# Performance work log

Hardware: AMD Instinct MI355X
Metric: run time of the kernel (lower is better)

The kernel has to match this reference:

```python
import jax, jax.numpy as jnp
from jax import lax
import numpy as np

LEVEL_HW = [(100, 100), (50, 50), (25, 25), (13, 13), (7, 7)]  # P3..P7 for 800x800 input
N, C, A, K, NCONV = 2, 256, 9, 80, 4
PRIOR_PROB = 0.01


def conv3x3(x, w, b):
    # x: (N,C,H,W), w: (O,I,3,3), stride 1, pad 1
    y = lax.conv_general_dilated(x, w, (1, 1), 'SAME',
                                 dimension_numbers=('NCHW', 'OIHW', 'NCHW'))
    return y + b[None, :, None, None]


def permute_to_N_HWA_K(t, k):
    # (N, A*k, H, W) -> (N, H*W*A, k), matching the torch helper
    n, _, h, w = t.shape
    return t.reshape(n, -1, k, h, w).transpose(0, 3, 4, 1, 2).reshape(n, -1, k)


def setup_inputs() -> dict:
    key = jax.random.key(0)
    ks = iter(jax.random.split(key, 64))
    inp = {}
    for i, (h, w) in enumerate(LEVEL_HW):
        inp[f"f{i}"] = jax.random.normal(next(ks), (N, C, h, w), jnp.float32)
    for pre in ("cls", "box"):
        for i in range(NCONV):
            inp[f"{pre}_w{i}"] = 0.01 * jax.random.normal(next(ks), (C, C, 3, 3), jnp.float32)
            inp[f"{pre}_b{i}"] = jnp.zeros((C,), jnp.float32)
    bias_value = -float(np.log((1.0 - PRIOR_PROB) / PRIOR_PROB))
    inp["cls_score_w"] = 0.01 * jax.random.normal(next(ks), (A * K, C, 3, 3), jnp.float32)
    inp["cls_score_b"] = jnp.full((A * K,), bias_value, jnp.float32)
    inp["box_pred_w"] = 0.01 * jax.random.normal(next(ks), (A * 4, C, 3, 3), jnp.float32)
    inp["box_pred_b"] = jnp.zeros((A * 4,), jnp.float32)
    return inp


def reference(f0, f1, f2, f3, f4,
              cls_w0, cls_b0, cls_w1, cls_b1, cls_w2, cls_b2, cls_w3, cls_b3,
              box_w0, box_b0, box_w1, box_b1, box_w2, box_b2, box_w3, box_b3,
              cls_score_w, cls_score_b, box_pred_w, box_pred_b):
    feats = [f0, f1, f2, f3, f4]
    cls_p = [(cls_w0, cls_b0), (cls_w1, cls_b1), (cls_w2, cls_b2), (cls_w3, cls_b3)]
    box_p = [(box_w0, box_b0), (box_w1, box_b1), (box_w2, box_b2), (box_w3, box_b3)]
    logits, boxes = [], []
    for f in feats:
        x = f
        for w, b in cls_p:
            x = jax.nn.relu(conv3x3(x, w, b))
        logits.append(permute_to_N_HWA_K(conv3x3(x, cls_score_w, cls_score_b), K))
        y = f
        for w, b in box_p:
            y = jax.nn.relu(conv3x3(y, w, b))
        boxes.append(permute_to_N_HWA_K(conv3x3(y, box_pred_w, box_pred_b), 4))
    # (N, R, K) and (N, R, 4) with R = sum_l Hl*Wl*A = 120087; concat on last dim
    return jnp.concatenate([jnp.concatenate(logits, 1), jnp.concatenate(boxes, 1)], axis=2)
```

## Files before the change

kernel.cpp:

```cpp
#include <hip/hip_runtime.h>


typedef __attribute__((ext_vector_type(8))) short short8;
typedef __attribute__((ext_vector_type(4))) float floatx4;

#define LVLTOT 14143

__device__ __forceinline__ unsigned short f2bf(float f) {
  unsigned int u = __float_as_uint(f);
  unsigned int r = (u + 0x7fffu + ((u >> 16) & 1u)) >> 16;
  return (unsigned short)r;
}

__device__ __forceinline__ void gload_lds16(const void* g, void* l) {
  __builtin_amdgcn_global_load_lds(
      (const __attribute__((address_space(1))) unsigned int*)g,
      (__attribute__((address_space(3))) unsigned int*)l, 16, 0, 0);
}

struct PrepArgs {
  const float* f[5];
  const float* w[10];
  unsigned short* wdst[10];
  int wblk_off[11];
  int cout[10];
  unsigned short* x0;
  unsigned short* bufA;
  unsigned short* bufB;
};

__global__ __launch_bounds__(256) void prep(PrepArgs A) {
  static const int Ht[5] = {100, 50, 25, 13, 7};
  static const int Wpt[5] = {102, 52, 27, 15, 9};
  static const int LOFFt[5] = {0, 10404, 13108, 13837, 14062};
  __shared__ float ts[32][33];
  const int bid = blockIdx.x;
  const int t = threadIdx.x;

  if (bid < 1090) {
    int sid = bid % 545, n = bid / 545;
    int l, h, wb;
    if (sid < 400)      { l = 0; h = sid >> 2; wb = sid & 3; }
    else if (sid < 500) { l = 1; h = (sid - 400) >> 1; wb = (sid - 400) & 1; }
    else if (sid < 525) { l = 2; h = sid - 500; wb = 0; }
    else if (sid < 538) { l = 3; h = sid - 525; wb = 0; }
    else                { l = 4; h = sid - 538; wb = 0; }
    const float* f = A.f[l];
    int H = Ht[l], W = H, Wp = Wpt[l], loff = LOFFt[l];
    int w0 = wb * 32;
    for (int s = 0; s < 8; s++) {
      int ch0 = s * 32;
      __syncthreads();
#pragma unroll
      for (int r4 = 0; r4 < 4; r4++) {
        int ch = ch0 + (t >> 5) + r4 * 8;
        int px = w0 + (t & 31);
        float v = 0.f;
        if (px < W) v = f[(((size_t)n * 256 + ch) * H + h) * W + px];
        ts[(t >> 5) + r4 * 8][t & 31] = v;
      }
      __syncthreads();
      int pxl = t >> 3, c4 = t & 7;
      if (w0 + pxl < W) {
        unsigned short pk[4];
#pragma unroll
        for (int k = 0; k < 4; k++) pk[k] = f2bf(ts[c4 * 4 + k][pxl]);
        *(unsigned long long*)(A.x0 +
            ((size_t)n * LVLTOT + loff + (size_t)(h + 1) * Wp + (w0 + pxl + 1)) *
                256 + ch0 + c4 * 4) = *(unsigned long long*)pk;
      }
    }
    return;
  }

  if (bid < 3970) {
    int b2 = bid - 1090;
    int tix = 0;
    while (b2 >= A.wblk_off[tix + 1]) tix++;
    int co = b2 - A.wblk_off[tix];
    int ci = t;
    bool valid = co < A.cout[tix];
    const float* w = A.w[tix];
    unsigned short* dst = A.wdst[tix];
    int cb = co >> 6, col = co & 63, chk = ci >> 5, qd = (ci >> 3) & 3, j = ci & 7;
#pragma unroll
    for (int tap = 0; tap < 9; tap++) {
      float v = valid ? w[((size_t)co * 256 + ci) * 9 + tap] : 0.f;
      dst[((((size_t)(cb * 8 + chk) * 9 + tap) * 4 + qd) * 64 + col) * 8 + j] =
          f2bf(v);
    }
    return;
  }

  {
    static const int BCUM[6] = {0, 404, 608, 712, 768, 800};
    int b3 = bid - 3970;
    int plane = b3 / 100;
    int item = (b3 % 100) * 256 + t;
    int pxi = item >> 5, oct = item & 31;
    if (pxi >= 800) return;
    int l = 0;
    while (pxi >= BCUM[l + 1]) l++;
    int j = pxi - BCUM[l];
    int Wp = Wpt[l];
    int r, c;
    if (j < Wp)            { r = 0; c = j; }
    else if (j < 2 * Wp)   { r = Wp - 1; c = j - Wp; }
    else { int k = j - 2 * Wp; r = 1 + (k >> 1); c = (k & 1) ? Wp - 1 : 0; }
    size_t px = (size_t)LOFFt[l] + (size_t)r * Wp + c;
    unsigned short* base = (plane < 4)
                               ? (A.bufA + (size_t)plane * LVLTOT * 256)
                               : (A.bufB + (size_t)(plane - 4) * LVLTOT * 256);
    floatx4 z;
    z[0] = z[1] = z[2] = z[3] = 0.f;
    *(floatx4*)(base + px * 256 + oct * 8) = z;
  }
}

__device__ __forceinline__ void decode_tile(int tile, int& l, int& h0, int& w0,
                                            int& H, int& W, int& Wp, int& loff) {
  const int Ht[5] = {100, 50, 25, 13, 7};
  const int Wpt[5] = {102, 52, 27, 15, 9};
  const int TXt[5] = {7, 4, 2, 1, 1};
  const int LOFFt[5] = {0, 10404, 13108, 13837, 14062};
  int tloc;
  if (tile < 49) { l = 0; tloc = tile; }
  else if (tile < 65) { l = 1; tloc = tile - 49; }
  else if (tile < 69) { l = 2; tloc = tile - 65; }
  else if (tile < 70) { l = 3; tloc = tile - 69; }
  else { l = 4; tloc = 0; }
  H = Ht[l]; W = H; Wp = Wpt[l]; loff = LOFFt[l];
  int ty = tloc / TXt[l], tx = tloc - ty * TXt[l];
  h0 = ty * 16; w0 = tx * 16;
}

#define CONV_MAIN_LOOP(INP, WBLOB, CB)                                         \
  {                                                                            \
    size_t xoff[6];                                                            \
    _Pragma("unroll") for (int g = 0; g < 6; g++) {                            \
      int px = g * 64 + lane;                                                  \
      int r = px / 18, c = px - r * 18;                                        \
      int hh = h0 + r; if (hh > Hpad - 1) hh = Hpad - 1;                       \
      int ww = w0 + c; if (ww > Wp - 1) ww = Wp - 1;                           \
      xoff[g] = ((size_t)hh * Wp + ww) * 256 + wv * 8;                         \
    }                                                                          \
    for (int ch = 0; ch < 8; ch++) {                                           \
      if (ch) __syncthreads();                                                 \
      const unsigned short* wsrc = (WBLOB) + ((size_t)((CB)*8 + ch)) * 18432;  \
      _Pragma("unroll") for (int i = 0; i < 9; i++)                            \
        gload_lds16(wsrc + i * 2048 + wv * 512 + lane * 8,                     \
                    lds_w + i * 2048 + wv * 512);                              \
      _Pragma("unroll") for (int g = 0; g < 6; g++)                            \
        gload_lds16((INP) + xoff[g] + ch * 32, lds_x + wv * 3072 + g * 512);   \
      __syncthreads();                                                         \
      const short8* xw = (const short8*)lds_w;                                 \
      const short8* xx = (const short8*)lds_x;                                 \
      _Pragma("unroll") for (int tdx = 0; tdx < 3; tdx++) {                    \
        short8 bfr[6];                                                         \
        _Pragma("unroll") for (int rw = 0; rw < 6; rw++)                       \
          bfr[rw] = xx[q * 384 + (wv * 4 + rw) * 18 + n16 + tdx];              \
        _Pragma("unroll") for (int tdy = 0; tdy < 3; tdy++) {                  \
          const int tap = tdy * 3 + tdx;                                       \
          _Pragma("unroll") for (int cc = 0; cc < 4; cc++) {                   \
            short8 afr = xw[(tap * 4 + q) * 64 + cc * 16 + n16];               \
            _Pragma("unroll") for (int rr = 0; rr < 4; rr++)                   \
              acc[cc][rr] = __builtin_amdgcn_mfma_f32_16x16x32_bf16(           \
                  afr, bfr[rr + tdy], acc[cc][rr], 0, 0, 0);                   \
          }                                                                    \
        }                                                                      \
      }                                                                        \
    }                                                                          \
  }

__global__ __launch_bounds__(256, 2) void conv_tower_mfma(
    const unsigned short* __restrict__ xin, unsigned short* __restrict__ xout,
    const unsigned short* __restrict__ wblob_cls,
    const unsigned short* __restrict__ wblob_box,
    const float* __restrict__ bias_cls, const float* __restrict__ bias_box,
    int in_n_stride, int in_tw_stride) {
  __shared__ __align__(16) unsigned short lds_w[18432];
  __shared__ __align__(16) unsigned short lds_x[12288];
  const int t = threadIdx.x, lane = t & 63, wv = t >> 6;
  const int q = lane >> 4, n16 = lane & 15;
  int l, h0, w0, H, W, Wp, loff;
  decode_tile(blockIdx.x, l, h0, w0, H, W, Wp, loff);
  const int Hpad = H + 2;
  const int cb = blockIdx.y;
  const int n = blockIdx.z >> 1, tw = blockIdx.z & 1;
  const unsigned short* wblob = tw ? wblob_box : wblob_cls;
  const float* bias = tw ? bias_box : bias_cls;
  const unsigned short* inp =
      xin + ((size_t)n * in_n_stride + (size_t)tw * in_tw_stride + loff) * 256;
  unsigned short* outp = xout + ((size_t)(n * 2 + tw) * LVLTOT + loff) * 256;

  floatx4 acc[4][4];
#pragma unroll
  for (int i = 0; i < 4; i++)
#pragma unroll
    for (int jj = 0; jj < 4; jj++) acc[i][jj] = (floatx4){0.f, 0.f, 0.f, 0.f};

  CONV_MAIN_LOOP(inp, wblob, cb)

#pragma unroll
  for (int cc = 0; cc < 4; cc++) {
    floatx4 bb = *(const floatx4*)(bias + cb * 64 + cc * 16 + q * 4);
#pragma unroll
    for (int rr = 0; rr < 4; rr++) {
      int h = h0 + wv * 4 + rr;
      int w_ = w0 + n16;
      if (h < H && w_ < W) {
        unsigned short pk[4];
#pragma unroll
        for (int rg = 0; rg < 4; rg++)
          pk[rg] = f2bf(fmaxf(acc[cc][rr][rg] + bb[rg], 0.f));
        size_t base =
            ((size_t)(h + 1) * Wp + (w_ + 1)) * 256 + cb * 64 + cc * 16 + q * 4;
        *(unsigned long long*)(outp + base) = *(unsigned long long*)pk;
      }
    }
  }
}

__global__ __launch_bounds__(256, 2) void conv_final_mfma(
    const unsigned short* __restrict__ xin, float* __restrict__ out,
    const unsigned short* __restrict__ wblob_cls,
    const unsigned short* __restrict__ wblob_box,
    const float* __restrict__ bias_cls, const float* __restrict__ bias_box) {
  __shared__ __align__(16) unsigned short lds_w[18432];
  __shared__ __align__(16) unsigned short lds_x[12288];
  const int t = threadIdx.x, lane = t & 63, wv = t >> 6;
  const int q = lane >> 4, n16 = lane & 15;
  int l, h0, w0, H, W, Wp, loff;
  decode_tile(blockIdx.x, l, h0, w0, H, W, Wp, loff);
  const int Hpad = H + 2;
  const int yb = blockIdx.y;
  const bool is_cls = yb < 12;
  const int cb = is_cls ? yb : 0;
  const int tw = is_cls ? 0 : 1;
  const int Cout = is_cls ? 720 : 36;
  const unsigned short* wblob = is_cls ? wblob_cls : wblob_box;
  const float* bias = is_cls ? bias_cls : bias_box;
  const int n = blockIdx.z;
  const int RB[5] = {0, 90000, 112500, 118125, 119646};
  const unsigned short* inp = xin + ((size_t)(n * 2 + tw) * LVLTOT + loff) * 256;

  floatx4 acc[4][4];
#pragma unroll
  for (int i = 0; i < 4; i++)
#pragma unroll
    for (int jj = 0; jj < 4; jj++) acc[i][jj] = (floatx4){0.f, 0.f, 0.f, 0.f};

  CONV_MAIN_LOOP(inp, wblob, cb)

#pragma unroll
  for (int cc = 0; cc < 4; cc++) {
    int co0 = cb * 64 + cc * 16 + q * 4;
    if (co0 >= Cout) continue;
    floatx4 bb = *(const floatx4*)(bias + co0);
    int a = is_cls ? (co0 / 80) : (co0 >> 2);
    int col0 = is_cls ? (co0 - a * 80) : 80;
#pragma unroll
    for (int rr = 0; rr < 4; rr++) {
      int h = h0 + wv * 4 + rr;
      int w_ = w0 + n16;
      if (h < H && w_ < W) {
        size_t ridx = (size_t)RB[l] + ((size_t)h * W + w_) * 9 + a;
        floatx4 v;
#pragma unroll
        for (int rg = 0; rg < 4; rg++) v[rg] = acc[cc][rr][rg] + bb[rg];
        *(floatx4*)(out + ((size_t)n * 120087 + ridx) * 84 + col0) = v;
      }
    }
  }
}

extern "C" void kernel_launch(void* const* d_in, const int* in_sizes, int n_in,
                              void* d_out, int out_size, void* d_ws,
                              size_t ws_size, hipStream_t stream) {
  char* ws = (char*)d_ws;
  unsigned short* bufB = (unsigned short*)(ws);
  unsigned short* X0 = (unsigned short*)(ws + 14482432);
  unsigned short* bufA = (unsigned short*)(ws + 28964864);
  unsigned short* tb[8];
  for (int i = 0; i < 8; i++)
    tb[i] = (unsigned short*)(ws + 57929728 + (size_t)i * 1179648);
  unsigned short* fb_cls = (unsigned short*)(ws + 67366912);
  unsigned short* fb_box = (unsigned short*)(ws + 70905856);

  float* out = (float*)d_out;

  PrepArgs pa;
  for (int i = 0; i < 5; i++) pa.f[i] = (const float*)d_in[i];
  for (int i = 0; i < 4; i++) {
    pa.w[i] = (const float*)d_in[5 + 2 * i];
    pa.w[4 + i] = (const float*)d_in[13 + 2 * i];
    pa.wdst[i] = tb[i];
    pa.wdst[4 + i] = tb[4 + i];
    pa.cout[i] = pa.cout[4 + i] = 256;
  }
  pa.w[8] = (const float*)d_in[21]; pa.wdst[8] = fb_cls; pa.cout[8] = 720;
  pa.w[9] = (const float*)d_in[23]; pa.wdst[9] = fb_box; pa.cout[9] = 36;
  int off = 0;
  for (int i = 0; i < 8; i++) { pa.wblk_off[i] = off; off += 256; }
  pa.wblk_off[8] = off; off += 768;
  pa.wblk_off[9] = off; off += 64;
  pa.wblk_off[10] = off;
  pa.x0 = X0;
  pa.bufA = bufA;
  pa.bufB = bufB;

  prep<<<dim3(4770), 256, 0, stream>>>(pa);

  const float *cls_b[4], *box_b[4];
  for (int i = 0; i < 4; i++) {
    cls_b[i] = (const float*)d_in[6 + 2 * i];
    box_b[i] = (const float*)d_in[14 + 2 * i];
  }

  dim3 gt(71, 4, 4);
  conv_tower_mfma<<<gt, 256, 0, stream>>>(X0, bufA, tb[0], tb[4], cls_b[0],
                                          box_b[0], LVLTOT, 0);
  conv_tower_mfma<<<gt, 256, 0, stream>>>(bufA, bufB, tb[1], tb[5], cls_b[1],
                                          box_b[1], 2 * LVLTOT, LVLTOT);
  conv_tower_mfma<<<gt, 256, 0, stream>>>(bufB, bufA, tb[2], tb[6], cls_b[2],
                                          box_b[2], 2 * LVLTOT, LVLTOT);
  conv_tower_mfma<<<gt, 256, 0, stream>>>(bufA, bufB, tb[3], tb[7], cls_b[3],
                                          box_b[3], 2 * LVLTOT, LVLTOT);

  conv_final_mfma<<<dim3(71, 13, 2), 256, 0, stream>>>(
      bufB, out, fb_cls, fb_box, (const float*)d_in[22], (const float*)d_in[24]);
}
```

Measured before the change: 638.5 us.

## Tile convs as packed 2x16 row segments across levels to cut padding waste

Replaces the fixed 16x16 spatial tiles per level with 2-row by 16-column segments. Each block packs 8 such segments, which can come from different pyramid levels, so partially empty tiles on the small levels and edges waste less compute. The input halo tile grows to 4x18 per segment, meaning each segment loads 72 pixels for 32 outputs. This raises LDS input usage and per-thread address setup, and the halo reuse is worse than with 16x16 tiles.

Measured after the change: 632.2 us. No clear change (-1.0%).

```diff
diff --git a/kernel.cpp b/kernel.cpp
--- a/kernel.cpp
+++ b/kernel.cpp
@@ -117,55 +117,62 @@
   }
 }
 
-__device__ __forceinline__ void decode_tile(int tile, int& l, int& h0, int& w0,
-                                            int& H, int& W, int& Wp, int& loff) {
-  const int Ht[5] = {100, 50, 25, 13, 7};
-  const int Wpt[5] = {102, 52, 27, 15, 9};
-  const int TXt[5] = {7, 4, 2, 1, 1};
-  const int LOFFt[5] = {0, 10404, 13108, 13837, 14062};
-  int tloc;
-  if (tile < 49) { l = 0; tloc = tile; }
-  else if (tile < 65) { l = 1; tloc = tile - 49; }
-  else if (tile < 69) { l = 2; tloc = tile - 65; }
-  else if (tile < 70) { l = 3; tloc = tile - 69; }
-  else { l = 4; tloc = 0; }
-  H = Ht[l]; W = H; Wp = Wpt[l]; loff = LOFFt[l];
-  int ty = tloc / TXt[l], tx = tloc - ty * TXt[l];
-  h0 = ty * 16; w0 = tx * 16;
-}
+__device__ __forceinline__ void decode_seg(int s, int& l, int& h0, int& w0,
+                                           int& H, int& Wp, int& loff) {
+  if (s < 350)      { l = 0; int hp = s / 7; w0 = (s - hp * 7) * 16; h0 = hp * 2;
+                      H = 100; Wp = 102; loff = 0; }
+  else if (s < 450) { l = 1; int r = s - 350; h0 = (r >> 2) * 2; w0 = (r & 3) * 16;
+                      H = 50; Wp = 52; loff = 10404; }
+  else if (s < 476) { l = 2; int r = s - 450; h0 = (r >> 1) * 2; w0 = (r & 1) * 16;
+                      H = 25; Wp = 27; loff = 13108; }
+  else if (s < 483) { l = 3; h0 = (s - 476) * 2; w0 = 0; H = 13; Wp = 15;
+                      loff = 13837; }
+  else              { l = 4; h0 = (s - 483) * 2; w0 = 0; H = 7; Wp = 9;
+                      loff = 14062; }
+}
+
+#define CONV_XPRE()                                                            \
+  int xsrc[9];                                                                 \
+  _Pragma("unroll") for (int k = 0; k < 9; k++) {                              \
+    int u = k * 256 + t;                                                       \
+    int qq = u / 576, rem = u - qq * 576;                                      \
+    int sl8 = rem / 72, rm2 = rem - sl8 * 72;                                  \
+    int r4 = rm2 / 18, c18 = rm2 - r4 * 18;                                    \
+    int sg = blockIdx.x * 8 + sl8; if (sg > 486) sg = 486;                     \
+    int l_, h0_, w0_, H_, Wp_, lo_;                                            \
+    decode_seg(sg, l_, h0_, w0_, H_, Wp_, lo_);                                \
+    int prow = h0_ + r4; if (prow > H_ + 1) prow = H_ + 1;                     \
+    int pcol = w0_ + c18; if (pcol > Wp_ - 1) pcol = Wp_ - 1;                  \
+    xsrc[k] = (lo_ + prow * Wp_ + pcol) * 256 + qq * 8;                        \
+  }
 
 #define CONV_MAIN_LOOP(INP, WBLOB, CB)                                         \
   {                                                                            \
-    size_t xoff[6];                                                            \
-    _Pragma("unroll") for (int g = 0; g < 6; g++) {                            \
-      int px = g * 64 + lane;                                                  \
-      int r = px / 18, c = px - r * 18;                                        \
-      int hh = h0 + r; if (hh > Hpad - 1) hh = Hpad - 1;                       \
-      int ww = w0 + c; if (ww > Wp - 1) ww = Wp - 1;                           \
-      xoff[g] = ((size_t)hh * Wp + ww) * 256 + wv * 8;                         \
-    }                                                                          \
-    for (int ch = 0; ch < 8; ch++) {                                           \
+    _Pragma("unroll 1") for (int ch = 0; ch < 8; ch++) {                       \
       if (ch) __syncthreads();                                                 \
       const unsigned short* wsrc = (WBLOB) + ((size_t)((CB)*8 + ch)) * 18432;  \
       _Pragma("unroll") for (int i = 0; i < 9; i++)                            \
         gload_lds16(wsrc + i * 2048 + wv * 512 + lane * 8,                     \
                     lds_w + i * 2048 + wv * 512);                              \
-      _Pragma("unroll") for (int g = 0; g < 6; g++)                            \
-        gload_lds16((INP) + xoff[g] + ch * 32, lds_x + wv * 3072 + g * 512);   \
+      _Pragma("unroll") for (int k = 0; k < 9; k++)                            \
+        gload_lds16((INP) + xsrc[k] + ch * 32,                                 \
+                    lds_x + (size_t)(k * 256 + wv * 64) * 8);                  \
       __syncthreads();                                                         \
       const short8* xw = (const short8*)lds_w;                                 \
       const short8* xx = (const short8*)lds_x;                                 \
       _Pragma("unroll") for (int tdx = 0; tdx < 3; tdx++) {                    \
-        short8 bfr[6];                                                         \
-        _Pragma("unroll") for (int rw = 0; rw < 6; rw++)                       \
-          bfr[rw] = xx[q * 384 + (wv * 4 + rw) * 18 + n16 + tdx];              \
+        short8 bfr[2][4];                                                      \
+        _Pragma("unroll") for (int sb = 0; sb < 2; sb++)                       \
+          _Pragma("unroll") for (int r = 0; r < 4; r++)                        \
+            bfr[sb][r] =                                                       \
+                xx[q * 576 + (wv * 2 + sb) * 72 + r * 18 + tdx + n16];         \
         _Pragma("unroll") for (int tdy = 0; tdy < 3; tdy++) {                  \
           const int tap = tdy * 3 + tdx;                                       \
           _Pragma("unroll") for (int cc = 0; cc < 4; cc++) {                   \
             short8 afr = xw[(tap * 4 + q) * 64 + cc * 16 + n16];               \
-            _Pragma("unroll") for (int rr = 0; rr < 4; rr++)                   \
-              acc[cc][rr] = __builtin_amdgcn_mfma_f32_16x16x32_bf16(           \
-                  afr, bfr[rr + tdy], acc[cc][rr], 0, 0, 0);                   \
+            _Pragma("unroll") for (int rg = 0; rg < 4; rg++)                   \
+              acc[cc][rg] = __builtin_amdgcn_mfma_f32_16x16x32_bf16(           \
+                  afr, bfr[rg >> 1][(rg & 1) + tdy], acc[cc][rg], 0, 0, 0);    \
           }                                                                    \
         }                                                                      \
       }                                                                        \
@@ -179,19 +186,16 @@
     const float* __restrict__ bias_cls, const float* __restrict__ bias_box,
     int in_n_stride, int in_tw_stride) {
   __shared__ __align__(16) unsigned short lds_w[18432];
-  __shared__ __align__(16) unsigned short lds_x[12288];
+  __shared__ __align__(16) unsigned short lds_x[18432];
   const int t = threadIdx.x, lane = t & 63, wv = t >> 6;
   const int q = lane >> 4, n16 = lane & 15;
-  int l, h0, w0, H, W, Wp, loff;
-  decode_tile(blockIdx.x, l, h0, w0, H, W, Wp, loff);
-  const int Hpad = H + 2;
   const int cb = blockIdx.y;
   const int n = blockIdx.z >> 1, tw = blockIdx.z & 1;
   const unsigned short* wblob = tw ? wblob_box : wblob_cls;
   const float* bias = tw ? bias_box : bias_cls;
   const unsigned short* inp =
-      xin + ((size_t)n * in_n_stride + (size_t)tw * in_tw_stride + loff) * 256;
-  unsigned short* outp = xout + ((size_t)(n * 2 + tw) * LVLTOT + loff) * 256;
+      xin + ((size_t)n * in_n_stride + (size_t)tw * in_tw_stride) * 256;
+  unsigned short* outp = xout + ((size_t)(n * 2 + tw) * LVLTOT) * 256;
 
   floatx4 acc[4][4];
 #pragma unroll
@@ -199,22 +203,27 @@
 #pragma unroll
     for (int jj = 0; jj < 4; jj++) acc[i][jj] = (floatx4){0.f, 0.f, 0.f, 0.f};
 
+  CONV_XPRE()
   CONV_MAIN_LOOP(inp, wblob, cb)
 
 #pragma unroll
-  for (int cc = 0; cc < 4; cc++) {
-    floatx4 bb = *(const floatx4*)(bias + cb * 64 + cc * 16 + q * 4);
-#pragma unroll
-    for (int rr = 0; rr < 4; rr++) {
-      int h = h0 + wv * 4 + rr;
-      int w_ = w0 + n16;
-      if (h < H && w_ < W) {
+  for (int rg = 0; rg < 4; rg++) {
+    int sg = blockIdx.x * 8 + wv * 2 + (rg >> 1);
+    if (sg > 486) sg = 486;
+    int l_, h0_, w0_, H_, Wp_, lo_;
+    decode_seg(sg, l_, h0_, w0_, H_, Wp_, lo_);
+    int h = h0_ + (rg & 1);
+    int w_ = w0_ + n16;
+    if (h < H_ && w_ < H_) {
+#pragma unroll
+      for (int cc = 0; cc < 4; cc++) {
+        floatx4 bb = *(const floatx4*)(bias + cb * 64 + cc * 16 + q * 4);
         unsigned short pk[4];
 #pragma unroll
-        for (int rg = 0; rg < 4; rg++)
-          pk[rg] = f2bf(fmaxf(acc[cc][rr][rg] + bb[rg], 0.f));
-        size_t base =
-            ((size_t)(h + 1) * Wp + (w_ + 1)) * 256 + cb * 64 + cc * 16 + q * 4;
+        for (int rgi = 0; rgi < 4; rgi++)
+          pk[rgi] = f2bf(fmaxf(acc[cc][rg][rgi] + bb[rgi], 0.f));
+        size_t base = ((size_t)lo_ + (size_t)(h + 1) * Wp_ + (w_ + 1)) * 256 +
+                      cb * 64 + cc * 16 + q * 4;
         *(unsigned long long*)(outp + base) = *(unsigned long long*)pk;
       }
     }
@@ -227,12 +236,9 @@
     const unsigned short* __restrict__ wblob_box,
     const float* __restrict__ bias_cls, const float* __restrict__ bias_box) {
   __shared__ __align__(16) unsigned short lds_w[18432];
-  __shared__ __align__(16) unsigned short lds_x[12288];
+  __shared__ __align__(16) unsigned short lds_x[18432];
   const int t = threadIdx.x, lane = t & 63, wv = t >> 6;
   const int q = lane >> 4, n16 = lane & 15;
-  int l, h0, w0, H, W, Wp, loff;
-  decode_tile(blockIdx.x, l, h0, w0, H, W, Wp, loff);
-  const int Hpad = H + 2;
   const int yb = blockIdx.y;
   const bool is_cls = yb < 12;
   const int cb = is_cls ? yb : 0;
@@ -242,7 +248,7 @@
   const float* bias = is_cls ? bias_cls : bias_box;
   const int n = blockIdx.z;
   const int RB[5] = {0, 90000, 112500, 118125, 119646};
-  const unsigned short* inp = xin + ((size_t)(n * 2 + tw) * LVLTOT + loff) * 256;
+  const unsigned short* inp = xin + ((size_t)(n * 2 + tw) * LVLTOT) * 256;
 
   floatx4 acc[4][4];
 #pragma unroll
@@ -250,25 +256,30 @@
 #pragma unroll
     for (int jj = 0; jj < 4; jj++) acc[i][jj] = (floatx4){0.f, 0.f, 0.f, 0.f};
 
+  CONV_XPRE()
   CONV_MAIN_LOOP(inp, wblob, cb)
 
 #pragma unroll
-  for (int cc = 0; cc < 4; cc++) {
-    int co0 = cb * 64 + cc * 16 + q * 4;
-    if (co0 >= Cout) continue;
-    floatx4 bb = *(const floatx4*)(bias + co0);
-    int a = is_cls ? (co0 / 80) : (co0 >> 2);
-    int col0 = is_cls ? (co0 - a * 80) : 80;
-#pragma unroll
-    for (int rr = 0; rr < 4; rr++) {
-      int h = h0 + wv * 4 + rr;
-      int w_ = w0 + n16;
-      if (h < H && w_ < W) {
-        size_t ridx = (size_t)RB[l] + ((size_t)h * W + w_) * 9 + a;
+  for (int rg = 0; rg < 4; rg++) {
+    int sg = blockIdx.x * 8 + wv * 2 + (rg >> 1);
+    if (sg > 486) sg = 486;
+    int l_, h0_, w0_, H_, Wp_, lo_;
+    decode_seg(sg, l_, h0_, w0_, H_, Wp_, lo_);
+    int h = h0_ + (rg & 1);
+    int w_ = w0_ + n16;
+    if (h < H_ && w_ < H_) {
+      size_t ridx = (size_t)RB[l_] + ((size_t)h * H_ + w_) * 9;
+#pragma unroll
+      for (int cc = 0; cc < 4; cc++) {
+        int co0 = cb * 64 + cc * 16 + q * 4;
+        if (co0 >= Cout) continue;
+        floatx4 bb = *(const floatx4*)(bias + co0);
+        int a = is_cls ? (co0 / 80) : (co0 >> 2);
+        int col0 = is_cls ? (co0 - a * 80) : 80;
         floatx4 v;
 #pragma unroll
-        for (int rg = 0; rg < 4; rg++) v[rg] = acc[cc][rr][rg] + bb[rg];
-        *(floatx4*)(out + ((size_t)n * 120087 + ridx) * 84 + col0) = v;
+        for (int rgi = 0; rgi < 4; rgi++) v[rgi] = acc[cc][rg][rgi] + bb[rgi];
+        *(floatx4*)(out + ((size_t)n * 120087 + ridx + a) * 84 + col0) = v;
       }
     }
   }
@@ -317,7 +328,7 @@
     box_b[i] = (const float*)d_in[14 + 2 * i];
   }
 
-  dim3 gt(71, 4, 4);
+  dim3 gt(61, 4, 4);
   conv_tower_mfma<<<gt, 256, 0, stream>>>(X0, bufA, tb[0], tb[4], cls_b[0],
                                           box_b[0], LVLTOT, 0);
   conv_tower_mfma<<<gt, 256, 0, stream>>>(bufA, bufB, tb[1], tb[5], cls_b[1],
@@ -327,6 +338,6 @@
   conv_tower_mfma<<<gt, 256, 0, stream>>>(bufA, bufB, tb[3], tb[7], cls_b[3],
                                           box_b[3], 2 * LVLTOT, LVLTOT);
 
-  conv_final_mfma<<<dim3(71, 13, 2), 256, 0, stream>>>(
+  conv_final_mfma<<<dim3(61, 13, 2), 256, 0, stream>>>(
       bufB, out, fb_cls, fb_box, (const float*)d_in[22], (const float*)d_in[24]);
 }
```
